# Kernel optimization log

Hardware: AMD Instinct MI355X
Metric: run time of the kernel (lower is better)

Reference implementation:

```python
import jax, jax.numpy as jnp
import numpy as np

EMBED_DIMS = 256
NUM_GROUPS = 8
NUM_LEVELS = 4
NUM_CAMS = 6
NUM_LEARNABLE_PTS = 6
FIX_SCALE = np.array([[0,0,0],[0.45,0,0],[-0.45,0,0],[0,0.45,0],[0,-0.45,0],[0,0,0.45],[0,0,-0.45]], dtype=np.float32)
NUM_PTS = len(FIX_SCALE) + NUM_LEARNABLE_PTS  # 13
GROUP_DIMS = EMBED_DIMS // NUM_GROUPS


def safe_sigmoid(x):
    return jax.nn.sigmoid(jnp.clip(x, -9.21, 9.21))


def get_rotation_matrix(q):
    # q: [..., 4] quaternion (w, x, y, z), normalized first (GaussianFormer convention)
    q = q / jnp.linalg.norm(q, axis=-1, keepdims=True)
    w, x, y, z = q[..., 0], q[..., 1], q[..., 2], q[..., 3]
    R = jnp.stack([
        jnp.stack([1 - 2 * (y * y + z * z), 2 * (x * y - w * z), 2 * (x * z + w * y)], axis=-1),
        jnp.stack([2 * (x * y + w * z), 1 - 2 * (x * x + z * z), 2 * (y * z - w * x)], axis=-1),
        jnp.stack([2 * (x * z - w * y), 2 * (y * z + w * x), 1 - 2 * (x * x + y * y)], axis=-1),
    ], axis=-2)
    return R  # [..., 3, 3]


def key_points_generator(anchor, instance_feature, W_learn, b_learn):
    bs, num_anchor = anchor.shape[:2]
    fix_scale = jnp.asarray(FIX_SCALE, anchor.dtype)  # [7, 3]
    scale = jnp.broadcast_to(fix_scale[None, None], (bs, num_anchor, fix_scale.shape[0], 3))
    learnable = safe_sigmoid((instance_feature @ W_learn + b_learn)
                             .reshape(bs, num_anchor, NUM_LEARNABLE_PTS, 3)) - 0.5
    scale = jnp.concatenate([scale, learnable], axis=-2)         # [bs, na, P, 3]
    gs_scales = anchor[..., None, 3:6]                           # [bs, na, 1, 3]
    key_points = scale * gs_scales                               # [bs, na, P, 3]
    rot_T = jnp.swapaxes(get_rotation_matrix(anchor[..., 6:10]), -1, -2)  # [bs, na, 3, 3]
    key_points = jnp.einsum('bnij,bnpj->bnpi', rot_T, key_points)
    return key_points + anchor[..., None, :3]                    # [bs, na, P, 3]


def project_points(key_points, projection_mat, image_wh):
    # key_points [bs, na, P, 3], projection_mat [bs, cams, 4, 4]
    ones = jnp.ones_like(key_points[..., :1])
    pts4 = jnp.concatenate([key_points, ones], axis=-1)          # [bs, na, P, 4]
    p2d = jnp.einsum('bcij,bnpj->bcnpi', projection_mat, pts4)   # [bs, cams, na, P, 4]
    p2d = p2d[..., :2] / jnp.maximum(p2d[..., 2:3], 1e-5)
    p2d = p2d / image_wh[:, :, None, None]
    return jnp.clip(p2d, 0.0, 0.9999)                            # [bs, cams, na, P, 2]


def bilinear_sample(feat, pts):
    # feat [bs, cams, C, H, W], pts [bs, P, cams, 2] normalized to [0,1]
    bs, cams, C, H, W = feat.shape
    x = pts[..., 0] * W - 0.5
    y = pts[..., 1] * H - 0.5
    x0 = jnp.floor(x); y0 = jnp.floor(y)
    wx = x - x0; wy = y - y0
    x0i = x0.astype(jnp.int32); y0i = y0.astype(jnp.int32)
    feat_f = jnp.transpose(feat, (0, 1, 3, 4, 2)).reshape(bs, cams, H * W, C)
    b_idx = jnp.arange(bs)[:, None, None]
    c_idx = jnp.arange(cams)[None, None, :]

    def gather(yy, xx):
        valid = (yy >= 0) & (yy < H) & (xx >= 0) & (xx < W)
        yc = jnp.clip(yy, 0, H - 1)
        xc = jnp.clip(xx, 0, W - 1)
        v = feat_f[b_idx, c_idx, yc * W + xc]                    # [bs, P, cams, C]
        return v * valid[..., None].astype(v.dtype)

    v00 = gather(y0i, x0i)
    v01 = gather(y0i, x0i + 1)
    v10 = gather(y0i + 1, x0i)
    v11 = gather(y0i + 1, x0i + 1)
    wx = wx[..., None]; wy = wy[..., None]
    return (v00 * (1 - wx) * (1 - wy) + v01 * wx * (1 - wy)
            + v10 * (1 - wx) * wy + v11 * wx * wy)               # [bs, P, cams, C]


def deformable_aggregate(feature_maps, points_2d, weights):
    # points_2d [bs, P, cams, 2]; weights [bs, P, cams, levels, groups]
    bs, P = points_2d.shape[:2]
    out = jnp.zeros((bs, P, NUM_GROUPS, GROUP_DIMS), points_2d.dtype)
    for l, feat in enumerate(feature_maps):
        samp = bilinear_sample(feat, points_2d)                  # [bs, P, cams, C]
        samp = samp.reshape(bs, P, feat.shape[1], NUM_GROUPS, GROUP_DIMS)
        out = out + jnp.einsum('bpcgd,bpcg->bpgd', samp, weights[:, :, :, l, :])
    return out.reshape(bs, P, EMBED_DIMS)


def _forward(pts3d, instance_feature, anchor, feat0, feat1, feat2, feat3,
             projection_mat, image_wh, W_learn, b_learn, W_wts, b_wts, W_out, b_out):
    bs, num_anchor = instance_feature.shape[:2]
    key_points = key_points_generator(anchor, instance_feature, W_learn, b_learn)
    # softmax weights over cams*levels*pts jointly, per group
    w = (instance_feature @ W_wts + b_wts).reshape(bs, num_anchor, -1, NUM_GROUPS)
    w = jax.nn.softmax(w, axis=-2)
    w = w.reshape(bs, num_anchor, NUM_CAMS, NUM_LEVELS, NUM_PTS, NUM_GROUPS)
    w = jnp.transpose(w, (0, 1, 4, 2, 3, 5)).reshape(bs, num_anchor * NUM_PTS, NUM_CAMS, NUM_LEVELS, NUM_GROUPS)
    p2d = project_points(key_points, projection_mat, image_wh)   # [bs, cams, na, P, 2]
    p2d = jnp.transpose(p2d, (0, 2, 3, 1, 4)).reshape(bs, num_anchor * NUM_PTS, NUM_CAMS, 2)
    feats = deformable_aggregate([feat0, feat1, feat2, feat3], p2d, w)
    feats = feats.reshape(bs, num_anchor, NUM_PTS, EMBED_DIMS).sum(axis=2)
    output = feats @ W_out + b_out
    return output + instance_feature


def setup_inputs() -> dict:
    key = jax.random.key(0)
    ks = jax.random.split(key, 16)
    bs, na = 1, 4096
    shapes = [(bs, 6, 256, 64, 176), (bs, 6, 256, 32, 88), (bs, 6, 256, 16, 44), (bs, 6, 256, 8, 22)]
    inp = {
        'pts3d': jax.random.normal(ks[0], (100000, 3), jnp.float32),
        'instance_feature': jax.random.normal(ks[1], (bs, na, EMBED_DIMS), jnp.float32),
        'anchor': jax.random.normal(ks[2], (bs, na, 11), jnp.float32),
        'feat0': jax.random.normal(ks[3], shapes[0], jnp.float32),
        'feat1': jax.random.normal(ks[4], shapes[1], jnp.float32),
        'feat2': jax.random.normal(ks[5], shapes[2], jnp.float32),
        'feat3': jax.random.normal(ks[6], shapes[3], jnp.float32),
        'projection_mat': jax.random.normal(ks[7], (bs, NUM_CAMS, 4, 4), jnp.float32),
        'image_wh': jnp.broadcast_to(jnp.array([704.0, 256.0], jnp.float32), (bs, NUM_CAMS, 2)),
        'W_learn': jax.random.normal(ks[8], (EMBED_DIMS, NUM_LEARNABLE_PTS * 3), jnp.float32) * 0.02,
        'b_learn': jnp.zeros((NUM_LEARNABLE_PTS * 3,), jnp.float32),
        'W_wts': jax.random.normal(ks[9], (EMBED_DIMS, NUM_GROUPS * NUM_CAMS * NUM_LEVELS * NUM_PTS), jnp.float32) * 0.02,
        'b_wts': jnp.zeros((NUM_GROUPS * NUM_CAMS * NUM_LEVELS * NUM_PTS,), jnp.float32),
        'W_out': jax.random.normal(ks[10], (EMBED_DIMS, EMBED_DIMS), jnp.float32) * 0.02,
        'b_out': jnp.zeros((EMBED_DIMS,), jnp.float32),
    }
    return inp


def reference(pts3d, instance_feature, anchor, feat0, feat1, feat2, feat3,
              projection_mat, image_wh, W_learn, b_learn, W_wts, b_wts, W_out, b_out):
    return _forward(pts3d, instance_feature, anchor, feat0, feat1, feat2, feat3,
                    projection_mat, image_wh, W_learn, b_learn, W_wts, b_wts, W_out, b_out)
```

## Files before the change

kernel.cpp:

```cpp
#include <hip/hip_runtime.h>
#include <math.h>


#define FT_L0 0
#define FT_L1 17301504
#define FT_L2 21626880
#define FT_L3 22708224
#define WS_LOGB 5744640
#define WS_FEATB 10856448
#define WS_LEARN 11380736
#define WS_AB 11454464
#define WS_BB 11978752
#define WS_WOB 12306432

typedef float v2f __attribute__((ext_vector_type(2)));
typedef __attribute__((ext_vector_type(8))) short bf16x8;
typedef __attribute__((ext_vector_type(4))) float f32x4;

__device__ const float FIXS[7][3] = {
    {0.f, 0.f, 0.f},  {0.45f, 0.f, 0.f}, {-0.45f, 0.f, 0.f}, {0.f, 0.45f, 0.f},
    {0.f, -0.45f, 0.f}, {0.f, 0.f, 0.45f}, {0.f, 0.f, -0.45f}};

__device__ __forceinline__ unsigned int f2bf(float f) {
  unsigned int u = __float_as_uint(f);
  u += 0x7fffu + ((u >> 16) & 1u);
  return u >> 16;
}
__device__ __forceinline__ float bf2f(unsigned short u) {
  return __uint_as_float(((unsigned int)u) << 16);
}

__global__ __launch_bounds__(256) void k_transpose_all(
    const float* __restrict__ f0, const float* __restrict__ f1,
    const float* __restrict__ f2, const float* __restrict__ f3,
    unsigned char* __restrict__ featF) {
  const int bx = blockIdx.x;
  const float* src;
  unsigned char* dst;
  int H, W, xt;
  if (bx < 6)       { src = f0; dst = featF + FT_L0; H = 64; W = 176; xt = bx * 32; }
  else if (bx < 9)  { src = f1; dst = featF + FT_L1; H = 32; W = 88;  xt = (bx - 6) * 32; }
  else if (bx < 11) { src = f2; dst = featF + FT_L2; H = 16; W = 44;  xt = (bx - 9) * 32; }
  else              { src = f3; dst = featF + FT_L3; H = 8;  W = 22;  xt = 0; }
  const int y = blockIdx.y;
  if (y >= H) return;
  __shared__ float tile[32][33];
  const int tid = threadIdx.x;
  const int i = tid & 31;
  const int j = tid >> 5;
  const int c = blockIdx.z >> 3;
  const int cht = (blockIdx.z & 7) * 32;
#pragma unroll
  for (int jj = j; jj < 32; jj += 8) {
    int x = xt + i;
    float v = 0.f;
    if (x < W) v = src[((c * 256 + cht + jj) * H + y) * W + x];
    tile[jj][i] = v;
  }
  __syncthreads();
  const int q = tid & 7;
  const int xw = tid >> 3;
  const int x = xt + xw;
  if (x < W) {
    const float v0 = tile[q * 4 + 0][xw];
    const float v1 = tile[q * 4 + 1][xw];
    const float v2 = tile[q * 4 + 2][xw];
    const float v3 = tile[q * 4 + 3][xw];
    int pk = __builtin_amdgcn_cvt_pk_fp8_f32(v0, v1, 0, false);
    pk = __builtin_amdgcn_cvt_pk_fp8_f32(v2, v3, pk, true);
    *(unsigned int*)(dst + (((c * H + y) * W + x) * 256) + cht + q * 4) =
        (unsigned int)pk;
  }
}

__global__ __launch_bounds__(256) void k_prep_pack(
    const float* __restrict__ iw, const float* __restrict__ Ww,
    const float* __restrict__ Wl, const float* __restrict__ Wo,
    unsigned short* __restrict__ Ab, unsigned short* __restrict__ Bb,
    unsigned short* __restrict__ Wob) {
  __shared__ unsigned short tile[32][33];
  const int tid = threadIdx.x;
  const int bx = blockIdx.x;
  if (bx < 1024) {
    const int i = bx * 256 + tid;
    const float4 v = ((const float4*)iw)[i];
    uint2 o;
    o.x = f2bf(v.x) | (f2bf(v.y) << 16);
    o.y = f2bf(v.z) | (f2bf(v.w) << 16);
    const int mtile = i >> 10;
    const int ml = (i >> 6) & 15;
    const int kk = (i & 63) >> 3;
    const int q = (i >> 1) & 3;
    const int j = (i & 1) * 4;
    *(uint2*)&Ab[mtile * 4096 + kk * 512 + q * 128 + ml * 8 + j] = o;
    return;
  }
  const int i = tid & 31;
  const int r = tid >> 5;
  if (bx < 1664) {
    const int idx = bx - 1024;
    const int j0 = (idx % 80) * 32;
    const int k0 = (idx / 80) * 32;
#pragma unroll
    for (int rr = r; rr < 32; rr += 8) {
      const int k = k0 + rr, jc = j0 + i;
      float v = 0.f;
      if (jc < 2496) v = Ww[k * 2496 + jc];
      else if (jc < 2514) v = Wl[k * 18 + (jc - 2496)];
      tile[rr][i] = (unsigned short)f2bf(v);
    }
    __syncthreads();
    const int jn = tid >> 3;
    const int kq = tid & 7;
    const int ncol = j0 + jn;
    const int k = k0 + kq * 4;
    const int ntile = ncol >> 4, mln = ncol & 15;
    const int kkn = k >> 5, qn = (k >> 3) & 3, jj = k & 7;
    unsigned int h0 = (unsigned int)tile[kq * 4 + 0][jn] |
                      ((unsigned int)tile[kq * 4 + 1][jn] << 16);
    unsigned int h1 = (unsigned int)tile[kq * 4 + 2][jn] |
                      ((unsigned int)tile[kq * 4 + 3][jn] << 16);
    *(uint2*)&Bb[ntile * 4096 + kkn * 512 + qn * 128 + mln * 8 + jj] =
        make_uint2(h0, h1);
  } else {
    const int idx = bx - 1664;
    const int j0 = (idx & 7) * 32;
    const int k0 = (idx >> 3) * 32;
#pragma unroll
    for (int rr = r; rr < 32; rr += 8)
      tile[rr][i] = (unsigned short)f2bf(Wo[(k0 + rr) * 256 + j0 + i]);
    __syncthreads();
#pragma unroll
    for (int rr = r; rr < 32; rr += 8)
      Wob[(j0 + rr) * 256 + k0 + i] = tile[i][rr];
  }
}

__global__ __launch_bounds__(256) void k_wts_mfma(
    const unsigned short* __restrict__ Ab, const unsigned short* __restrict__ Bb,
    const float* __restrict__ b_wts, const float* __restrict__ b_learn,
    unsigned short* __restrict__ logitsB, float* __restrict__ learn) {
  const int tid = threadIdx.x;
  const int w = tid >> 6, lane = tid & 63;
  const int ml = lane & 15, q = lane >> 4;
  const int n0 = blockIdx.x * 64;
  const int m0 = blockIdx.y * 64;
  f32x4 acc[4] = {{0.f, 0.f, 0.f, 0.f}, {0.f, 0.f, 0.f, 0.f},
                  {0.f, 0.f, 0.f, 0.f}, {0.f, 0.f, 0.f, 0.f}};
  const unsigned short* Ap = Ab + (blockIdx.y * 4 + w) * 4096 + lane * 8;
  const unsigned short* Bp = Bb + blockIdx.x * 4 * 4096 + lane * 8;
#pragma unroll
  for (int kk = 0; kk < 8; ++kk) {
    const bf16x8 a = *(const bf16x8*)(Ap + kk * 512);
#pragma unroll
    for (int nt = 0; nt < 4; ++nt) {
      const bf16x8 b = *(const bf16x8*)(Bp + nt * 4096 + kk * 512);
      acc[nt] = __builtin_amdgcn_mfma_f32_16x16x32_bf16(a, b, acc[nt], 0, 0, 0);
    }
  }
  const int rowb = m0 + w * 16 + q * 4;
#pragma unroll
  for (int nt = 0; nt < 4; ++nt) {
    const int col = n0 + nt * 16 + ml;
    if (col < 2496) {
      const float b = b_wts[col];
#pragma unroll
      for (int r = 0; r < 4; ++r)
        logitsB[(rowb + r) * 2496 + col] = (unsigned short)f2bf(acc[nt][r] + b);
    } else if (col < 2514) {
      const float b = b_learn[col - 2496];
#pragma unroll
      for (int r = 0; r < 4; ++r) {
        float v = fminf(fmaxf(acc[nt][r] + b, -9.21f), 9.21f);
        learn[(rowb + r) * 18 + (col - 2496)] = 1.f / (1.f + expf(-v)) - 0.5f;
      }
    }
  }
}

__device__ __forceinline__ void fma16(const uint4 u, const float s, v2f* acc) {
  const v2f w = {s, s};
  acc[0] += __builtin_amdgcn_cvt_pk_f32_fp8((int)u.x, false) * w;
  acc[1] += __builtin_amdgcn_cvt_pk_f32_fp8((int)u.x, true) * w;
  acc[2] += __builtin_amdgcn_cvt_pk_f32_fp8((int)u.y, false) * w;
  acc[3] += __builtin_amdgcn_cvt_pk_f32_fp8((int)u.y, true) * w;
  acc[4] += __builtin_amdgcn_cvt_pk_f32_fp8((int)u.z, false) * w;
  acc[5] += __builtin_amdgcn_cvt_pk_f32_fp8((int)u.z, true) * w;
  acc[6] += __builtin_amdgcn_cvt_pk_f32_fp8((int)u.w, false) * w;
  acc[7] += __builtin_amdgcn_cvt_pk_f32_fp8((int)u.w, true) * w;
}

__global__ __launch_bounds__(256, 8) void k_sample(
    const float* __restrict__ anchor, const unsigned short* __restrict__ logitsB,
    const float* __restrict__ learn_g, const unsigned char* __restrict__ featF,
    const float* __restrict__ proj, const float* __restrict__ wh,
    unsigned short* __restrict__ featsB) {
  const int n = blockIdx.x;
  const int tid = threadIdx.x;
  const int lane = tid & 63;
  const int wave = tid >> 6;
  __shared__ unsigned short s_w[8 * 328];
  __shared__ float s_p2d[78][2];
  __shared__ float s_learn[18];
  __shared__ union SmpLds {
    struct { int4 off[320]; float4 wt[320]; } tab;
    float red[4][256];
  } u;

  for (int i = tid; i < 2496; i += 256) {
    const int s = i >> 3, g = i & 7;
    const int c = s / 52;
    const int r = s - c * 52;
    const int l = r / 13;
    const int p = r - l * 13;
    s_w[g * 328 + (p * 6 + c) * 4 + l] = logitsB[n * 2496 + i];
  }
  if (tid < 64) s_w[(tid >> 3) * 328 + 312 + (tid & 7)] = 0;
  if (tid < 18) s_learn[tid] = learn_g[n * 18 + tid];
  __syncthreads();

#pragma unroll
  for (int gg = 0; gg < 2; ++gg) {
    unsigned short* row = &s_w[(wave * 2 + gg) * 328];
    float l[5];
    float mx = -1e30f;
#pragma unroll
    for (int i = 0; i < 5; ++i) {
      const int s = lane + i * 64;
      l[i] = (s < 312) ? bf2f(row[s]) : -1e30f;
      mx = fmaxf(mx, l[i]);
    }
    for (int off = 32; off; off >>= 1) mx = fmaxf(mx, __shfl_xor(mx, off));
    float sum = 0.f;
#pragma unroll
    for (int i = 0; i < 5; ++i) {
      l[i] = __expf(l[i] - mx);
      sum += l[i];
    }
    for (int off = 32; off; off >>= 1) sum += __shfl_xor(sum, off);
    const float inv = 1.f / sum;
#pragma unroll
    for (int i = 0; i < 5; ++i) {
      const int s = lane + i * 64;
      if (s < 312) row[s] = (unsigned short)f2bf(l[i] * inv);
    }
  }

  if (tid < 78) {
    const int p = tid / 6, c = tid % 6;
    const float* an = anchor + n * 11;
    float qw = an[6], qx = an[7], qy = an[8], qz = an[9];
    const float qinv = 1.f / sqrtf(qw * qw + qx * qx + qy * qy + qz * qz);
    qw *= qinv; qx *= qinv; qy *= qinv; qz *= qinv;
    const float R00 = 1.f - 2.f * (qy * qy + qz * qz), R01 = 2.f * (qx * qy - qw * qz), R02 = 2.f * (qx * qz + qw * qy);
    const float R10 = 2.f * (qx * qy + qw * qz), R11 = 1.f - 2.f * (qx * qx + qz * qz), R12 = 2.f * (qy * qz - qw * qx);
    const float R20 = 2.f * (qx * qz - qw * qy), R21 = 2.f * (qy * qz + qw * qx), R22 = 1.f - 2.f * (qx * qx + qy * qy);
    float s0, s1, s2;
    if (p < 7) {
      s0 = FIXS[p][0]; s1 = FIXS[p][1]; s2 = FIXS[p][2];
    } else {
      const int b = (p - 7) * 3;
      s0 = s_learn[b]; s1 = s_learn[b + 1]; s2 = s_learn[b + 2];
    }
    const float vx = s0 * an[3], vy = s1 * an[4], vz = s2 * an[5];
    const float kx = R00 * vx + R10 * vy + R20 * vz + an[0];
    const float ky = R01 * vx + R11 * vy + R21 * vz + an[1];
    const float kz = R02 * vx + R12 * vy + R22 * vz + an[2];
    const float* P = proj + c * 16;
    const float h0 = P[0] * kx + P[1] * ky + P[2] * kz + P[3];
    const float h1 = P[4] * kx + P[5] * ky + P[6] * kz + P[7];
    const float h2 = P[8] * kx + P[9] * ky + P[10] * kz + P[11];
    const float zz = fmaxf(h2, 1e-5f);
    float px = h0 / zz / wh[c * 2 + 0];
    float py = h1 / zz / wh[c * 2 + 1];
    px = fminf(fmaxf(px, 0.f), 0.9999f);
    py = fminf(fmaxf(py, 0.f), 0.9999f);
    s_p2d[tid][0] = px;
    s_p2d[tid][1] = py;
  }
  __syncthreads();

  {
    constexpr int LBB[4] = {FT_L0, FT_L1, FT_L2, FT_L3};
    constexpr int CSB[4] = {2883584, 720896, 180224, 45056};
    for (int t = tid; t < 320; t += 256) {
      const int pc = t >> 2, l = t & 3;
      if (pc >= 78) {
        u.tab.off[t] = make_int4(0, 0, 0, 0);
        u.tab.wt[t] = make_float4(0.f, 0.f, 0.f, 0.f);
        continue;
      }
      const int c = pc % 6;
      const int H = 64 >> l, W = 176 >> l;
      const float fx = s_p2d[pc][0] * (float)W - 0.5f;
      const float fy = s_p2d[pc][1] * (float)H - 0.5f;
      const float x0f = floorf(fx), y0f = floorf(fy);
      const float wx = fx - x0f, wy = fy - y0f;
      const int x0 = (int)x0f, y0 = (int)y0f;
      const float mx0 = (x0 >= 0) ? 1.f : 0.f;
      const float mx1 = (x0 + 1 < W) ? 1.f : 0.f;
      const float my0 = (y0 >= 0) ? 1.f : 0.f;
      const float my1 = (y0 + 1 < H) ? 1.f : 0.f;
      const int cx0 = max(x0, 0), cx1 = min(x0 + 1, W - 1);
      const int cy0 = max(y0, 0), cy1 = min(y0 + 1, H - 1);
      const int base = LBB[l] + c * CSB[l];
      int4 o;
      o.x = base + (cy0 * W + cx0) * 256;
      o.y = base + (cy0 * W + cx1) * 256;
      o.z = base + (cy1 * W + cx0) * 256;
      o.w = base + (cy1 * W + cx1) * 256;
      u.tab.off[t] = o;
      float4 w4;
      w4.x = (1.f - wx) * (1.f - wy) * mx0 * my0;
      w4.y = wx * (1.f - wy) * mx1 * my0;
      w4.z = (1.f - wx) * wy * mx0 * my1;
      w4.w = wx * wy * mx1 * my1;
      u.tab.wt[t] = w4;
    }
  }
  __syncthreads();

  const int q = lane >> 4;
  const int ql = lane & 15;
  const int chb = ql * 16;
  const int g = ql >> 1;
  v2f acc[8];
#pragma unroll
  for (int k = 0; k < 8; ++k) acc[k] = (v2f){0.f, 0.f};
  const unsigned char* fb = featF;
  const unsigned short* wrow = &s_w[g * 328];
  const int pcb = wave * 4 + q;
#pragma unroll
  for (int it = 0; it < 5; ++it) {
    const int pc = pcb + it * 16;
    const int t0 = pc * 4;
    const uint2 wq = *(const uint2*)&wrow[t0];
    float wgl[4];
    wgl[0] = __uint_as_float(wq.x << 16);
    wgl[1] = __uint_as_float(wq.x & 0xffff0000u);
    wgl[2] = __uint_as_float(wq.y << 16);
    wgl[3] = __uint_as_float(wq.y & 0xffff0000u);
#pragma unroll
    for (int l4 = 0; l4 < 4; ++l4) {
      const int t = t0 + l4;
      const int4 o = u.tab.off[t];
      const float4 bw = u.tab.wt[t];
      const float wg = wgl[l4];
      const uint4 u0 = *(const uint4*)(fb + (o.x + chb));
      const uint4 u1 = *(const uint4*)(fb + (o.y + chb));
      const uint4 u2 = *(const uint4*)(fb + (o.z + chb));
      const uint4 u3 = *(const uint4*)(fb + (o.w + chb));
      fma16(u0, bw.x * wg, acc);
      fma16(u1, bw.y * wg, acc);
      fma16(u2, bw.z * wg, acc);
      fma16(u3, bw.w * wg, acc);
    }
  }
#pragma unroll
  for (int k = 0; k < 8; ++k) {
    v2f b;
    b.x = __shfl_xor(acc[k].x, 16);
    b.y = __shfl_xor(acc[k].y, 16);
    acc[k] += b;
    b.x = __shfl_xor(acc[k].x, 32);
    b.y = __shfl_xor(acc[k].y, 32);
    acc[k] += b;
  }
  __syncthreads();
  if (lane < 16) {
    float* dst = &u.red[wave][ql * 16];
    *(float4*)(dst + 0)  = make_float4(acc[0].x, acc[0].y, acc[1].x, acc[1].y);
    *(float4*)(dst + 4)  = make_float4(acc[2].x, acc[2].y, acc[3].x, acc[3].y);
    *(float4*)(dst + 8)  = make_float4(acc[4].x, acc[4].y, acc[5].x, acc[5].y);
    *(float4*)(dst + 12) = make_float4(acc[6].x, acc[6].y, acc[7].x, acc[7].y);
  }
  __syncthreads();
  {
    const float sum = u.red[0][tid] + u.red[1][tid] + u.red[2][tid] + u.red[3][tid];
    featsB[n * 256 + tid] = (unsigned short)f2bf(sum);
  }
}

__global__ __launch_bounds__(256) void k_out_mfma(
    const unsigned short* __restrict__ Ab, const unsigned short* __restrict__ Bb,
    const float* __restrict__ bias, const float* __restrict__ resid,
    float* __restrict__ out) {
  const int tid = threadIdx.x;
  const int w = tid >> 6, lane = tid & 63;
  const int ml = lane & 15, q = lane >> 4;
  const int n0 = blockIdx.x * 64;
  const int m0 = blockIdx.y * 64;
  f32x4 acc[4] = {{0.f, 0.f, 0.f, 0.f}, {0.f, 0.f, 0.f, 0.f},
                  {0.f, 0.f, 0.f, 0.f}, {0.f, 0.f, 0.f, 0.f}};
  const unsigned short* Ap = Ab + (m0 + w * 16 + ml) * 256 + q * 8;
  const unsigned short* Bp = Bb + (n0 + ml) * 256 + q * 8;
#pragma unroll
  for (int kk = 0; kk < 8; ++kk) {
    const bf16x8 a = *(const bf16x8*)(Ap + kk * 32);
#pragma unroll
    for (int nt = 0; nt < 4; ++nt) {
      const bf16x8 b = *(const bf16x8*)(Bp + nt * 16 * 256 + kk * 32);
      acc[nt] = __builtin_amdgcn_mfma_f32_16x16x32_bf16(a, b, acc[nt], 0, 0, 0);
    }
  }
  const int rowb = m0 + w * 16 + q * 4;
#pragma unroll
  for (int nt = 0; nt < 4; ++nt) {
    const int col = n0 + nt * 16 + ml;
    const float b = bias[col];
#pragma unroll
    for (int r = 0; r < 4; ++r) {
      const int row = rowb + r;
      out[row * 256 + col] = acc[nt][r] + b + resid[row * 256 + col];
    }
  }
}

extern "C" void kernel_launch(void* const* d_in, const int* in_sizes, int n_in,
                              void* d_out, int out_size, void* d_ws, size_t ws_size,
                              hipStream_t stream) {
  (void)in_sizes; (void)n_in; (void)out_size; (void)ws_size;
  const float* iw      = (const float*)d_in[1];
  const float* anchor  = (const float*)d_in[2];
  const float* f0      = (const float*)d_in[3];
  const float* f1      = (const float*)d_in[4];
  const float* f2      = (const float*)d_in[5];
  const float* f3      = (const float*)d_in[6];
  const float* proj    = (const float*)d_in[7];
  const float* wh      = (const float*)d_in[8];
  const float* W_learn = (const float*)d_in[9];
  const float* b_learn = (const float*)d_in[10];
  const float* W_wts   = (const float*)d_in[11];
  const float* b_wts   = (const float*)d_in[12];
  const float* W_out   = (const float*)d_in[13];
  const float* b_out   = (const float*)d_in[14];
  float* out = (float*)d_out;
  float* ws = (float*)d_ws;
  unsigned char*  featF   = (unsigned char*)ws;
  unsigned short* logitsB = (unsigned short*)(ws + WS_LOGB);
  unsigned short* featsB  = (unsigned short*)(ws + WS_FEATB);
  float*          learn   = ws + WS_LEARN;
  unsigned short* Ab      = (unsigned short*)(ws + WS_AB);
  unsigned short* Bb      = (unsigned short*)(ws + WS_BB);
  unsigned short* Wob     = (unsigned short*)(ws + WS_WOB);

  k_transpose_all<<<dim3(12, 64, 48), 256, 0, stream>>>(f0, f1, f2, f3, featF);
  k_prep_pack<<<1728, 256, 0, stream>>>(iw, W_wts, W_learn, W_out, Ab, Bb, Wob);
  k_wts_mfma<<<dim3(40, 64), 256, 0, stream>>>(Ab, Bb, b_wts, b_learn, logitsB, learn);
  k_sample<<<4096, 256, 0, stream>>>(anchor, logitsB, learn, featF, proj, wh, featsB);
  k_out_mfma<<<dim3(4, 64), 256, 0, stream>>>(featsB, Wob, b_out, iw, out);
}
```

Baseline: 272.0 us.

## Pre-permute weight-logit columns in GEMM output and merge staging kernels

Folds the (group, cam, level, point) permutation into the packed B matrix and bias, so the weight GEMM writes logits already in the sampler's layout. The GEMM epilogue now stages each tile through LDS and writes 16-byte rows, and the sampler loads its logits with contiguous uint4 copies instead of a scalar scatter. The feature transpose and weight-packing kernels are merged into one launch, removing a launch and letting their blocks overlap. In exchange there is an extra LDS round-trip and a barrier in the GEMM epilogue, plus more complex index math in the packing stage.

```diff
diff --git a/kernel.cpp b/kernel.cpp
--- a/kernel.cpp
+++ b/kernel.cpp
@@ -12,6 +12,7 @@
 #define WS_AB 11454464
 #define WS_BB 11978752
 #define WS_WOB 12306432
+#define WS_BIASP 12339200
 
 typedef float v2f __attribute__((ext_vector_type(2)));
 typedef __attribute__((ext_vector_type(8))) short bf16x8;
@@ -30,57 +31,61 @@
   return __uint_as_float(((unsigned int)u) << 16);
 }
 
-__global__ __launch_bounds__(256) void k_transpose_all(
+__global__ __launch_bounds__(256) void k_stage(
     const float* __restrict__ f0, const float* __restrict__ f1,
     const float* __restrict__ f2, const float* __restrict__ f3,
-    unsigned char* __restrict__ featF) {
-  const int bx = blockIdx.x;
-  const float* src;
-  unsigned char* dst;
-  int H, W, xt;
-  if (bx < 6)       { src = f0; dst = featF + FT_L0; H = 64; W = 176; xt = bx * 32; }
-  else if (bx < 9)  { src = f1; dst = featF + FT_L1; H = 32; W = 88;  xt = (bx - 6) * 32; }
-  else if (bx < 11) { src = f2; dst = featF + FT_L2; H = 16; W = 44;  xt = (bx - 9) * 32; }
-  else              { src = f3; dst = featF + FT_L3; H = 8;  W = 22;  xt = 0; }
-  const int y = blockIdx.y;
-  if (y >= H) return;
-  __shared__ float tile[32][33];
-  const int tid = threadIdx.x;
-  const int i = tid & 31;
-  const int j = tid >> 5;
-  const int c = blockIdx.z >> 3;
-  const int cht = (blockIdx.z & 7) * 32;
-#pragma unroll
-  for (int jj = j; jj < 32; jj += 8) {
-    int x = xt + i;
-    float v = 0.f;
-    if (x < W) v = src[((c * 256 + cht + jj) * H + y) * W + x];
-    tile[jj][i] = v;
-  }
-  __syncthreads();
-  const int q = tid & 7;
-  const int xw = tid >> 3;
-  const int x = xt + xw;
-  if (x < W) {
-    const float v0 = tile[q * 4 + 0][xw];
-    const float v1 = tile[q * 4 + 1][xw];
-    const float v2 = tile[q * 4 + 2][xw];
-    const float v3 = tile[q * 4 + 3][xw];
-    int pk = __builtin_amdgcn_cvt_pk_fp8_f32(v0, v1, 0, false);
-    pk = __builtin_amdgcn_cvt_pk_fp8_f32(v2, v3, pk, true);
-    *(unsigned int*)(dst + (((c * H + y) * W + x) * 256) + cht + q * 4) =
-        (unsigned int)pk;
-  }
-}
-
-__global__ __launch_bounds__(256) void k_prep_pack(
+    unsigned char* __restrict__ featF,
     const float* __restrict__ iw, const float* __restrict__ Ww,
     const float* __restrict__ Wl, const float* __restrict__ Wo,
+    const float* __restrict__ b_wts,
     unsigned short* __restrict__ Ab, unsigned short* __restrict__ Bb,
-    unsigned short* __restrict__ Wob) {
-  __shared__ unsigned short tile[32][33];
+    unsigned short* __restrict__ Wob, float* __restrict__ biasP) {
+  __shared__ union {
+    float tf[32][33];
+    unsigned short tu[32][33];
+  } sm;
   const int tid = threadIdx.x;
-  const int bx = blockIdx.x;
+  const int bid = blockIdx.x;
+  if (bid < 36864) {
+    const int bx = bid % 12;
+    const int y = (bid / 12) & 63;
+    const int bz = bid / 768;
+    const float* src;
+    unsigned char* dst;
+    int H, W, xt;
+    if (bx < 6)       { src = f0; dst = featF + FT_L0; H = 64; W = 176; xt = bx * 32; }
+    else if (bx < 9)  { src = f1; dst = featF + FT_L1; H = 32; W = 88;  xt = (bx - 6) * 32; }
+    else if (bx < 11) { src = f2; dst = featF + FT_L2; H = 16; W = 44;  xt = (bx - 9) * 32; }
+    else              { src = f3; dst = featF + FT_L3; H = 8;  W = 22;  xt = 0; }
+    if (y >= H) return;
+    const int i = tid & 31;
+    const int j = tid >> 5;
+    const int c = bz >> 3;
+    const int cht = (bz & 7) * 32;
+#pragma unroll
+    for (int jj = j; jj < 32; jj += 8) {
+      int x = xt + i;
+      float v = 0.f;
+      if (x < W) v = src[((c * 256 + cht + jj) * H + y) * W + x];
+      sm.tf[jj][i] = v;
+    }
+    __syncthreads();
+    const int q = tid & 7;
+    const int xw = tid >> 3;
+    const int x = xt + xw;
+    if (x < W) {
+      const float v0 = sm.tf[q * 4 + 0][xw];
+      const float v1 = sm.tf[q * 4 + 1][xw];
+      const float v2 = sm.tf[q * 4 + 2][xw];
+      const float v3 = sm.tf[q * 4 + 3][xw];
+      int pk = __builtin_amdgcn_cvt_pk_fp8_f32(v0, v1, 0, false);
+      pk = __builtin_amdgcn_cvt_pk_fp8_f32(v2, v3, pk, true);
+      *(unsigned int*)(dst + (((c * H + y) * W + x) * 256) + cht + q * 4) =
+          (unsigned int)pk;
+    }
+    return;
+  }
+  const int bx = bid - 36864;
   if (bx < 1024) {
     const int i = bx * 256 + tid;
     const float4 v = ((const float4*)iw)[i];
@@ -91,8 +96,18 @@
     const int ml = (i >> 6) & 15;
     const int kk = (i & 63) >> 3;
     const int q = (i >> 1) & 3;
-    const int j = (i & 1) * 4;
-    *(uint2*)&Ab[mtile * 4096 + kk * 512 + q * 128 + ml * 8 + j] = o;
+    const int jj = (i & 1) * 4;
+    *(uint2*)&Ab[mtile * 4096 + kk * 512 + q * 128 + ml * 8 + jj] = o;
+    return;
+  }
+  if (bx >= 1728) {
+    const int jcol = (bx - 1728) * 256 + tid;
+    if (jcol < 2496) {
+      const int g = jcol & 7, s = jcol >> 3;
+      const int c = s / 52, r2 = s - c * 52;
+      const int l = r2 / 13, p = r2 - l * 13;
+      biasP[g * 312 + (p * 6 + c) * 4 + l] = b_wts[jcol];
+    }
     return;
   }
   const int i = tid & 31;
@@ -107,39 +122,51 @@
       float v = 0.f;
       if (jc < 2496) v = Ww[k * 2496 + jc];
       else if (jc < 2514) v = Wl[k * 18 + (jc - 2496)];
-      tile[rr][i] = (unsigned short)f2bf(v);
+      sm.tu[rr][i] = (unsigned short)f2bf(v);
     }
     __syncthreads();
     const int jn = tid >> 3;
     const int kq = tid & 7;
-    const int ncol = j0 + jn;
-    const int k = k0 + kq * 4;
-    const int ntile = ncol >> 4, mln = ncol & 15;
-    const int kkn = k >> 5, qn = (k >> 3) & 3, jj = k & 7;
-    unsigned int h0 = (unsigned int)tile[kq * 4 + 0][jn] |
-                      ((unsigned int)tile[kq * 4 + 1][jn] << 16);
-    unsigned int h1 = (unsigned int)tile[kq * 4 + 2][jn] |
-                      ((unsigned int)tile[kq * 4 + 3][jn] << 16);
-    *(uint2*)&Bb[ntile * 4096 + kkn * 512 + qn * 128 + mln * 8 + jj] =
-        make_uint2(h0, h1);
+    const int jc = j0 + jn;
+    if (jc < 2514) {
+      int colp;
+      if (jc < 2496) {
+        const int g = jc & 7, s = jc >> 3;
+        const int c = s / 52, r2 = s - c * 52;
+        const int l = r2 / 13, p = r2 - l * 13;
+        colp = g * 312 + (p * 6 + c) * 4 + l;
+      } else {
+        colp = jc;
+      }
+      const int k = k0 + kq * 4;
+      const int ntile = colp >> 4, mln = colp & 15;
+      const int kkn = k >> 5, qn = (k >> 3) & 3, jj = k & 7;
+      unsigned int h0 = (unsigned int)sm.tu[kq * 4 + 0][jn] |
+                        ((unsigned int)sm.tu[kq * 4 + 1][jn] << 16);
+      unsigned int h1 = (unsigned int)sm.tu[kq * 4 + 2][jn] |
+                        ((unsigned int)sm.tu[kq * 4 + 3][jn] << 16);
+      *(uint2*)&Bb[ntile * 4096 + kkn * 512 + qn * 128 + mln * 8 + jj] =
+          make_uint2(h0, h1);
+    }
   } else {
     const int idx = bx - 1664;
     const int j0 = (idx & 7) * 32;
     const int k0 = (idx >> 3) * 32;
 #pragma unroll
     for (int rr = r; rr < 32; rr += 8)
-      tile[rr][i] = (unsigned short)f2bf(Wo[(k0 + rr) * 256 + j0 + i]);
+      sm.tu[rr][i] = (unsigned short)f2bf(Wo[(k0 + rr) * 256 + j0 + i]);
     __syncthreads();
 #pragma unroll
     for (int rr = r; rr < 32; rr += 8)
-      Wob[(j0 + rr) * 256 + k0 + i] = tile[i][rr];
+      Wob[(j0 + rr) * 256 + k0 + i] = sm.tu[i][rr];
   }
 }
 
 __global__ __launch_bounds__(256) void k_wts_mfma(
     const unsigned short* __restrict__ Ab, const unsigned short* __restrict__ Bb,
-    const float* __restrict__ b_wts, const float* __restrict__ b_learn,
-    unsigned short* __restrict__ logitsB, float* __restrict__ learn) {
+    const float* __restrict__ biasP, const float* __restrict__ b_learn,
+    unsigned short* __restrict__ logitsP, float* __restrict__ learn) {
+  __shared__ __align__(16) unsigned short t64[64][88];
   const int tid = threadIdx.x;
   const int w = tid >> 6, lane = tid & 63;
   const int ml = lane & 15, q = lane >> 4;
@@ -158,21 +185,32 @@
       acc[nt] = __builtin_amdgcn_mfma_f32_16x16x32_bf16(a, b, acc[nt], 0, 0, 0);
     }
   }
-  const int rowb = m0 + w * 16 + q * 4;
-#pragma unroll
-  for (int nt = 0; nt < 4; ++nt) {
-    const int col = n0 + nt * 16 + ml;
-    if (col < 2496) {
-      const float b = b_wts[col];
+  if (blockIdx.x < 39) {
+    const int wr = w * 16 + q * 4;
+#pragma unroll
+    for (int nt = 0; nt < 4; ++nt) {
+      const float b = biasP[n0 + nt * 16 + ml];
 #pragma unroll
       for (int r = 0; r < 4; ++r)
-        logitsB[(rowb + r) * 2496 + col] = (unsigned short)f2bf(acc[nt][r] + b);
-    } else if (col < 2514) {
-      const float b = b_learn[col - 2496];
-#pragma unroll
-      for (int r = 0; r < 4; ++r) {
-        float v = fminf(fmaxf(acc[nt][r] + b, -9.21f), 9.21f);
-        learn[(rowb + r) * 18 + (col - 2496)] = 1.f / (1.f + expf(-v)) - 0.5f;
+        t64[wr + r][nt * 16 + ml] = (unsigned short)f2bf(acc[nt][r] + b);
+    }
+    __syncthreads();
+    const int row = tid >> 2, cq = tid & 3;
+    unsigned short* drow = logitsP + (m0 + row) * 2496 + n0;
+    *(uint4*)(drow + cq * 8) = *(const uint4*)&t64[row][cq * 8];
+    *(uint4*)(drow + 32 + cq * 8) = *(const uint4*)&t64[row][32 + cq * 8];
+  } else {
+    const int rowb = m0 + w * 16 + q * 4;
+#pragma unroll
+    for (int nt = 0; nt < 4; ++nt) {
+      const int col = n0 + nt * 16 + ml;
+      if (col < 2514) {
+        const float b = b_learn[col - 2496];
+#pragma unroll
+        for (int r = 0; r < 4; ++r) {
+          float v = fminf(fmaxf(acc[nt][r] + b, -9.21f), 9.21f);
+          learn[(rowb + r) * 18 + (col - 2496)] = 1.f / (1.f + expf(-v)) - 0.5f;
+        }
       }
     }
   }
@@ -191,7 +229,7 @@
 }
 
 __global__ __launch_bounds__(256, 8) void k_sample(
-    const float* __restrict__ anchor, const unsigned short* __restrict__ logitsB,
+    const float* __restrict__ anchor, const unsigned short* __restrict__ logitsP,
     const float* __restrict__ learn_g, const unsigned char* __restrict__ featF,
     const float* __restrict__ proj, const float* __restrict__ wh,
     unsigned short* __restrict__ featsB) {
@@ -199,7 +237,7 @@
   const int tid = threadIdx.x;
   const int lane = tid & 63;
   const int wave = tid >> 6;
-  __shared__ unsigned short s_w[8 * 328];
+  __shared__ __align__(16) unsigned short s_w[8 * 328];
   __shared__ float s_p2d[78][2];
   __shared__ float s_learn[18];
   __shared__ union SmpLds {
@@ -207,13 +245,12 @@
     float red[4][256];
   } u;
 
-  for (int i = tid; i < 2496; i += 256) {
-    const int s = i >> 3, g = i & 7;
-    const int c = s / 52;
-    const int r = s - c * 52;
-    const int l = r / 13;
-    const int p = r - l * 13;
-    s_w[g * 328 + (p * 6 + c) * 4 + l] = logitsB[n * 2496 + i];
+  {
+    const uint4* lp = (const uint4*)(logitsP + (size_t)n * 2496);
+    for (int i = tid; i < 312; i += 256) {
+      const int g = i / 39;
+      ((uint4*)s_w)[g * 41 + (i - g * 39)] = lp[i];
+    }
   }
   if (tid < 64) s_w[(tid >> 3) * 328 + 312 + (tid & 7)] = 0;
   if (tid < 18) s_learn[tid] = learn_g[n * 18 + tid];
@@ -437,16 +474,17 @@
   float* out = (float*)d_out;
   float* ws = (float*)d_ws;
   unsigned char*  featF   = (unsigned char*)ws;
-  unsigned short* logitsB = (unsigned short*)(ws + WS_LOGB);
+  unsigned short* logitsP = (unsigned short*)(ws + WS_LOGB);
   unsigned short* featsB  = (unsigned short*)(ws + WS_FEATB);
   float*          learn   = ws + WS_LEARN;
   unsigned short* Ab      = (unsigned short*)(ws + WS_AB);
   unsigned short* Bb      = (unsigned short*)(ws + WS_BB);
   unsigned short* Wob     = (unsigned short*)(ws + WS_WOB);
-
-  k_transpose_all<<<dim3(12, 64, 48), 256, 0, stream>>>(f0, f1, f2, f3, featF);
-  k_prep_pack<<<1728, 256, 0, stream>>>(iw, W_wts, W_learn, W_out, Ab, Bb, Wob);
-  k_wts_mfma<<<dim3(40, 64), 256, 0, stream>>>(Ab, Bb, b_wts, b_learn, logitsB, learn);
-  k_sample<<<4096, 256, 0, stream>>>(anchor, logitsB, learn, featF, proj, wh, featsB);
+  float*          biasP   = ws + WS_BIASP;
+
+  k_stage<<<38603, 256, 0, stream>>>(f0, f1, f2, f3, featF, iw, W_wts, W_learn,
+                                     W_out, b_wts, Ab, Bb, Wob, biasP);
+  k_wts_mfma<<<dim3(40, 64), 256, 0, stream>>>(Ab, Bb, biasP, b_learn, logitsP, learn);
+  k_sample<<<4096, 256, 0, stream>>>(anchor, logitsP, learn, featF, proj, wh, featsB);
   k_out_mfma<<<dim3(4, 64), 256, 0, stream>>>(featsB, Wob, b_out, iw, out);
 }
```

Result: no change. 271.8 us (-0.1%).
